# Kernel optimization log

Hardware: AMD Instinct MI355X
Metric: run time of the kernel (lower is better)

The kernel has to match this reference:

```python
import jax, jax.numpy as jnp
import numpy as np

DIM, D_STATE, D_CONV, EXPAND = 128, 16, 4, 2
D_INNER = EXPAND * DIM          # 256
DT_RANK = (DIM + 15) // 16      # 8
HIDDEN = int(DIM * 4.0)         # 512


def layer_norm(x, w, b, eps=1e-5):
    mu = x.mean(-1, keepdims=True)
    var = ((x - mu) ** 2).mean(-1, keepdims=True)
    return (x - mu) * jax.lax.rsqrt(var + eps) * w + b


def mamba(x, in_proj_w, conv_w, conv_b, x_proj_w, dt_proj_w, dt_proj_b, A_log, D, out_proj_w):
    # x: [B, L, dim]
    B, L, _ = x.shape
    xz = jnp.einsum('bld,ed->ble', x, in_proj_w)          # [B,L,2*Din]
    xc, z = jnp.split(xz, 2, axis=-1)                     # [B,L,Din] each
    # causal depthwise conv1d over L
    xcT = jnp.swapaxes(xc, 1, 2)                          # [B,Din,L]
    xcT = jax.lax.conv_general_dilated(
        xcT, conv_w, window_strides=(1,), padding=[(D_CONV - 1, 0)],
        dimension_numbers=('NCH', 'OIH', 'NCH'), feature_group_count=D_INNER)
    xc = jax.nn.silu(jnp.swapaxes(xcT, 1, 2) + conv_b)    # [B,L,Din]
    # input-dependent SSM parameters
    x_dbl = jnp.einsum('bld,ed->ble', xc, x_proj_w)       # [B,L,dt_rank+2N]
    dt, Bm, Cm = jnp.split(x_dbl, [DT_RANK, DT_RANK + D_STATE], axis=-1)
    delta = jax.nn.softplus(jnp.einsum('blr,dr->bld', dt, dt_proj_w) + dt_proj_b)  # [B,L,Din]
    A = -jnp.exp(A_log)                                   # [Din,N]
    deltaA = jnp.exp(delta[..., None] * A)                # [B,L,Din,N]
    deltaBu = (delta * xc)[..., None] * Bm[:, :, None, :] # [B,L,Din,N]
    # linear recurrence over L: h = deltaA*h + deltaBu ; y = <h, C>
    def step(h, inp):
        dA, dBu, c = inp
        h = dA * h + dBu                                  # [B,Din,N]
        return h, jnp.einsum('bdn,bn->bd', h, c)
    h0 = jnp.zeros((B, D_INNER, D_STATE), deltaA.dtype)
    _, ys = jax.lax.scan(step, h0, (jnp.swapaxes(deltaA, 0, 1),
                                    jnp.swapaxes(deltaBu, 0, 1),
                                    jnp.swapaxes(Cm, 0, 1)))
    y = jnp.swapaxes(ys, 0, 1) + xc * D                   # [B,L,Din]
    y = y * jax.nn.silu(z)
    return jnp.einsum('bld,od->blo', y, out_proj_w)       # [B,L,dim]


def mlp(x, H, W, fc1_w, fc1_b, dw_w, dw_b, fc2_w, fc2_b):
    B, L, _ = x.shape
    T = L // (H * W)
    h = jnp.einsum('bld,hd->blh', x, fc1_w) + fc1_b       # [B,L,hidden]
    hs = h.reshape(B * T, H, W, HIDDEN)                   # NHWC
    hs = jax.lax.conv_general_dilated(
        hs, dw_w, window_strides=(1, 1), padding='SAME',
        dimension_numbers=('NHWC', 'HWIO', 'NHWC'), feature_group_count=HIDDEN) + dw_b
    h = jax.nn.gelu(hs.reshape(B, L, HIDDEN), approximate=False)
    return jnp.einsum('blh,oh->blo', h, fc2_w) + fc2_b


def setup_inputs() -> dict:
    key = jax.random.key(0)
    ks = jax.random.split(key, 20)
    s = 0.02
    return {
        'x_in': jax.random.normal(ks[0], (2, 8, DIM, 32, 32), jnp.float32),
        'norm1_w': jnp.ones((DIM,), jnp.float32),
        'norm1_b': jnp.zeros((DIM,), jnp.float32),
        'in_proj_w': jax.random.normal(ks[1], (2 * D_INNER, DIM), jnp.float32) * s,
        'conv_w': jax.random.normal(ks[2], (D_INNER, 1, D_CONV), jnp.float32) * s,
        'conv_b': jnp.zeros((D_INNER,), jnp.float32),
        'x_proj_w': jax.random.normal(ks[3], (DT_RANK + 2 * D_STATE, D_INNER), jnp.float32) * s,
        'dt_proj_w': jax.random.normal(ks[4], (D_INNER, DT_RANK), jnp.float32) * s,
        'dt_proj_b': jax.random.uniform(ks[5], (D_INNER,), jnp.float32, -4.0, -2.0),
        'A_log': jnp.log(jnp.broadcast_to(jnp.arange(1, D_STATE + 1, dtype=jnp.float32), (D_INNER, D_STATE))),
        'D': jnp.ones((D_INNER,), jnp.float32),
        'out_proj_w': jax.random.normal(ks[6], (DIM, D_INNER), jnp.float32) * s,
        'norm2_w': jnp.ones((DIM,), jnp.float32),
        'norm2_b': jnp.zeros((DIM,), jnp.float32),
        'fc1_w': jax.random.normal(ks[7], (HIDDEN, DIM), jnp.float32) * s,
        'fc1_b': jnp.zeros((HIDDEN,), jnp.float32),
        'dw_w': jax.random.normal(ks[8], (3, 3, 1, HIDDEN), jnp.float32) * s,
        'dw_b': jnp.zeros((HIDDEN,), jnp.float32),
        'fc2_w': jax.random.normal(ks[9], (DIM, HIDDEN), jnp.float32) * s,
        'fc2_b': jnp.zeros((DIM,), jnp.float32),
    }


def reference(x_in, norm1_w, norm1_b, in_proj_w, conv_w, conv_b, x_proj_w,
              dt_proj_w, dt_proj_b, A_log, D, out_proj_w, norm2_w, norm2_b,
              fc1_w, fc1_b, dw_w, dw_b, fc2_w, fc2_b):
    B, T, C, H, W = x_in.shape
    L = T * H * W
    x = jnp.transpose(x_in, (0, 1, 3, 4, 2)).reshape(B, L, C)
    shortcut = x
    xn = layer_norm(x, norm1_w, norm1_b)
    mamba_args = (in_proj_w, conv_w, conv_b, x_proj_w, dt_proj_w, dt_proj_b, A_log, D, out_proj_w)
    out = mamba(xn, *mamba_args) + jnp.flip(mamba(jnp.flip(xn, 1), *mamba_args), 1)
    x = shortcut + out
    x = x + mlp(layer_norm(x, norm2_w, norm2_b), H, W, fc1_w, fc1_b, dw_w, dw_b, fc2_w, fc2_b)
    return jnp.transpose(x.reshape(B, T, H, W, C), (0, 1, 4, 2, 3))
```

## Files before the change

### kernel.cpp

```cpp
#include <hip/hip_runtime.h>
#include <math.h>

#define BB 2
#define HWSZ 1024
#define LL 8192
#define MM 16384
#define DMODEL 128
#define DIN 256
#define NST 16
#define CH 32
#define NCH 256

typedef __attribute__((ext_vector_type(8))) short bf16x8;
typedef __attribute__((ext_vector_type(4))) float f32x4;

__device__ __forceinline__ float siluf(float x){ return x/(1.f+__expf(-x)); }
__device__ __forceinline__ unsigned short f2bf(float x){
  unsigned u = __float_as_uint(x);
  unsigned r = (u + 0x7fffu + ((u>>16)&1u)) >> 16;
  return (unsigned short)r;
}
__device__ __forceinline__ float bf2f(unsigned short h){ return __uint_as_float(((unsigned)h)<<16); }
__device__ __forceinline__ float softplusf(float x){
  return fmaxf(x,0.f) + __logf(1.f + __expf(-fabsf(x)));
}

__global__ __launch_bounds__(256) void k_tln(const float* __restrict__ in,
    const float* __restrict__ w, const float* __restrict__ b,
    float* __restrict__ x_t, unsigned short* __restrict__ xn){
  __shared__ float st[128][33];
  int bt = blockIdx.y, hw0 = blockIdx.x*32;
  int t = threadIdx.x;
  int tx = t & 31, ty = t >> 5;
  #pragma unroll
  for (int j=0;j<16;j++){
    int c = ty + j*8;
    st[c][tx] = in[((size_t)(bt*DMODEL + c))*HWSZ + hw0 + tx];
  }
  __syncthreads();
  int wv = t >> 6, l = t & 63;
  float2 wgt = *(const float2*)(w + 2*l);
  float2 bia = *(const float2*)(b + 2*l);
  #pragma unroll
  for (int p=0;p<8;p++){
    int tok = p*4 + wv;
    float e0 = st[2*l][tok], e1 = st[2*l+1][tok];
    float s = e0+e1, sq = e0*e0+e1*e1;
    #pragma unroll
    for (int off=32; off>=1; off>>=1){ s += __shfl_xor(s,off); sq += __shfl_xor(sq,off); }
    float mu = s*(1.f/128.f);
    float var = sq*(1.f/128.f) - mu*mu;
    float rs = rsqrtf(var + 1e-5f);
    size_t tg = (size_t)bt*HWSZ + hw0 + tok;
    *(float2*)(x_t + tg*DMODEL + 2*l) = make_float2(e0,e1);
    ushort2 o;
    o.x = f2bf((e0-mu)*rs*wgt.x + bia.x);
    o.y = f2bf((e1-mu)*rs*wgt.y + bia.y);
    *(ushort2*)(xn + tg*DMODEL + 2*l) = o;
  }
}

__global__ void k_prep_weights(const float* __restrict__ ipw, const float* __restrict__ xpw,
                               const float* __restrict__ dtw, const float* __restrict__ opw,
                               const float* __restrict__ f1w, const float* __restrict__ f2w,
                               unsigned short* __restrict__ wb){
  int i = blockIdx.x*256 + threadIdx.x;
  const int T0=65536, T1=T0+81920, T2=T1+32768, T3=T2+65536, T4=T3+65536;
  if (i >= T4) return;
  float v;
  if (i < T0) v = ipw[i];
  else if (i < T1){
    int j = i - T0; int row = j >> 8; int col = j & 255;
    if (row < 256){
      float acc = 0.f;
      #pragma unroll
      for (int r=0;r<8;r++) acc += dtw[row*8+r]*xpw[r*256+col];
      v = acc;
    } else if (row < 288) v = xpw[(8 + row-256)*256 + col];
    else v = 0.f;
  }
  else if (i < T2) v = opw[i - T1];
  else if (i < T3) v = f1w[i - T2];
  else v = f2w[i - T3];
  wb[i] = f2bf(v);
}

template<int BM, int BN, int WM, int WN, int EPI>
__global__ __launch_bounds__(256) void k_mgemm(
    const unsigned short* __restrict__ A, const unsigned short* __restrict__ W,
    void* __restrict__ Cout, const float* __restrict__ bias,
    const float* __restrict__ add, unsigned short* __restrict__ C2,
    const float* __restrict__ lnw, const float* __restrict__ lnb,
    int M, int N, int K){
  constexpr int BK = 64;
  constexpr int TM = WM/16, TN = WN/16;
  constexpr int NWN = BN/WN;
  static_assert((BM/WM)*(BN/WN) == 4, "4 waves");
  __shared__ unsigned short As[BM*BK];
  __shared__ unsigned short Bs[BN*BK];
  const int tid = threadIdx.x;
  const int w = tid >> 6, l = tid & 63;
  const int m0 = blockIdx.y*BM, n0 = blockIdx.x*BN;
  const int wm = w / NWN, wn = w % NWN;
  f32x4 acc[TM][TN];
  #pragma unroll
  for (int i=0;i<TM;i++)
    #pragma unroll
    for (int j=0;j<TN;j++) acc[i][j] = (f32x4){0.f,0.f,0.f,0.f};
  const int lrow = l >> 3;
  const int lswz = ((l & 7) ^ lrow) * 8;
  const int rl = l & 15;
  const int gh = l >> 4;
  const int sx7 = l & 7;
  for (int k0 = 0; k0 < K; k0 += BK){
    #pragma unroll
    for (int r0 = 0; r0 < BM; r0 += 32){
      int rr = r0 + w*8;
      const unsigned short* gp = A + (size_t)(m0 + rr + lrow)*K + k0 + lswz;
      __builtin_amdgcn_global_load_lds(
        (const __attribute__((address_space(1))) unsigned int*)gp,
        (__attribute__((address_space(3))) unsigned int*)(As + rr*BK), 16, 0, 0);
    }
    #pragma unroll
    for (int r0 = 0; r0 < BN; r0 += 32){
      int rr = r0 + w*8;
      const unsigned short* gp = W + (size_t)(n0 + rr + lrow)*K + k0 + lswz;
      __builtin_amdgcn_global_load_lds(
        (const __attribute__((address_space(1))) unsigned int*)gp,
        (__attribute__((address_space(3))) unsigned int*)(Bs + rr*BK), 16, 0, 0);
    }
    __syncthreads();
    #pragma unroll
    for (int kk = 0; kk < 2; kk++){
      const int slot = ((kk*4 + gh) ^ sx7) * 8;
      bf16x8 af[TM], bfr[TN];
      #pragma unroll
      for (int i=0;i<TM;i++)
        af[i] = *(const bf16x8*)(As + (wm*WM + i*16 + rl)*BK + slot);
      #pragma unroll
      for (int j=0;j<TN;j++)
        bfr[j] = *(const bf16x8*)(Bs + (wn*WN + j*16 + rl)*BK + slot);
      #pragma unroll
      for (int i=0;i<TM;i++)
        #pragma unroll
        for (int j=0;j<TN;j++)
          acc[i][j] = __builtin_amdgcn_mfma_f32_16x16x32_bf16(af[i], bfr[j], acc[i][j], 0,0,0);
    }
    __syncthreads();
  }
  if constexpr (EPI == 5){
    __shared__ float st2[64][65];
    __syncthreads();
    #pragma unroll
    for (int i=0;i<TM;i++){
      #pragma unroll
      for (int j=0;j<TN;j++){
        #pragma unroll
        for (int r=0;r<4;r++){
          int rloc = wm*WM + i*16 + (gh<<2) + r;
          int cloc = wn*WN + j*16 + rl;
          int row = m0 + rloc, col = n0 + cloc;
          st2[rloc][cloc] = acc[i][j][r] + bias[col] + add[(size_t)row*N + col];
        }
      }
    }
    __syncthreads();
    int bt = m0 >> 10, hw0 = m0 & 1023;
    float* outp = (float*)Cout;
    #pragma unroll
    for (int it=0; it<16; it++){
      int colL = it*4 + w;
      outp[((size_t)(bt*DMODEL + n0 + colL))*HWSZ + hw0 + l] = st2[l][colL];
    }
  } else if constexpr (EPI == 6){
    __shared__ float st2[64][129];
    __syncthreads();
    #pragma unroll
    for (int i=0;i<TM;i++){
      #pragma unroll
      for (int j=0;j<TN;j++){
        #pragma unroll
        for (int r=0;r<4;r++){
          int rloc = wm*WM + i*16 + (gh<<2) + r;
          int cloc = wn*WN + j*16 + rl;
          int row = m0 + rloc;
          float v = acc[i][j][r] + add[(size_t)row*128 + cloc];
          st2[rloc][cloc] = v;
          ((float*)Cout)[(size_t)row*128 + cloc] = v;
        }
      }
    }
    __syncthreads();
    int rr = tid >> 2, part = tid & 3;
    float s = 0.f, sq = 0.f;
    #pragma unroll
    for (int q=0;q<32;q++){
      float v = st2[rr][part*32+q];
      s += v; sq += v*v;
    }
    s += __shfl_xor(s,1); s += __shfl_xor(s,2);
    sq += __shfl_xor(sq,1); sq += __shfl_xor(sq,2);
    float mu = s*(1.f/128.f);
    float var = sq*(1.f/128.f) - mu*mu;
    float rs = rsqrtf(var + 1e-5f);
    int row = m0 + rr;
    #pragma unroll
    for (int q=0;q<32;q+=2){
      int col = part*32 + q;
      ushort2 o;
      o.x = f2bf((st2[rr][col]  -mu)*rs*lnw[col]   + lnb[col]);
      o.y = f2bf((st2[rr][col+1]-mu)*rs*lnw[col+1] + lnb[col+1]);
      *(ushort2*)(C2 + (size_t)row*128 + col) = o;
    }
  } else {
    #pragma unroll
    for (int i=0;i<TM;i++){
      #pragma unroll
      for (int j=0;j<TN;j++){
        #pragma unroll
        for (int r=0;r<4;r++){
          int row = m0 + wm*WM + i*16 + (gh<<2) + r;
          int col = n0 + wn*WN + j*16 + rl;
          float v = acc[i][j][r];
          if (EPI == 0){
            ((unsigned short*)Cout)[(size_t)row*N + col] = f2bf(v);
          } else if (EPI == 1){
            ((unsigned short*)Cout)[(size_t)row*N + col] = f2bf(v + bias[col]);
          } else if (EPI == 2){
            if (col < 256){
              ((unsigned short*)Cout)[(size_t)row*256 + col] = f2bf(softplusf(v + bias[col]));
            } else if (col < 288){
              C2[(size_t)row*32 + (col-256)] = f2bf(v);
            }
          } else if (EPI == 3){
            ((float*)Cout)[(size_t)row*N + col] = v + add[(size_t)row*N + col];
          }
        }
      }
    }
  }
}

__global__ void k_conv1d(const unsigned short* __restrict__ xz, const float* __restrict__ cw,
                         const float* __restrict__ cb, unsigned short* __restrict__ xcf,
                         unsigned short* __restrict__ xcb){
  int idx = blockIdx.x*256 + threadIdx.x;
  int d4 = (idx & 63)*4;
  int ml = idx >> 6;
  int b = ml >> 13, l = ml & (LL-1);
  float4 t0 = *(const float4*)(cw + (size_t)(d4+0)*4);
  float4 t1 = *(const float4*)(cw + (size_t)(d4+1)*4);
  float4 t2 = *(const float4*)(cw + (size_t)(d4+2)*4);
  float4 t3 = *(const float4*)(cw + (size_t)(d4+3)*4);
  float wk[4][4];
  wk[0][0]=t0.x; wk[1][0]=t0.y; wk[2][0]=t0.z; wk[3][0]=t0.w;
  wk[0][1]=t1.x; wk[1][1]=t1.y; wk[2][1]=t1.z; wk[3][1]=t1.w;
  wk[0][2]=t2.x; wk[1][2]=t2.y; wk[2][2]=t2.z; wk[3][2]=t2.w;
  wk[0][3]=t3.x; wk[1][3]=t3.y; wk[2][3]=t3.z; wk[3][3]=t3.w;
  float4 bv = *(const float4*)(cb + d4);
  const unsigned short* base = xz + (size_t)b*LL*512 + d4;
  float4 af = {0,0,0,0};
  #pragma unroll
  for (int k=0;k<4;k++){
    int lp = l-3+k;
    if (lp>=0){
      ushort4 u = *(const ushort4*)(base + (size_t)lp*512);
      af.x += wk[k][0]*bf2f(u.x); af.y += wk[k][1]*bf2f(u.y);
      af.z += wk[k][2]*bf2f(u.z); af.w += wk[k][3]*bf2f(u.w);
    }
  }
  ushort4 of;
  of.x = f2bf(siluf(af.x+bv.x)); of.y = f2bf(siluf(af.y+bv.y));
  of.z = f2bf(siluf(af.z+bv.z)); of.w = f2bf(siluf(af.w+bv.w));
  *(ushort4*)(xcf + (size_t)ml*DIN + d4) = of;
  float4 ab = {0,0,0,0};
  #pragma unroll
  for (int k=0;k<4;k++){
    int lp = l+3-k;
    if (lp<LL){
      ushort4 u = *(const ushort4*)(base + (size_t)lp*512);
      ab.x += wk[k][0]*bf2f(u.x); ab.y += wk[k][1]*bf2f(u.y);
      ab.z += wk[k][2]*bf2f(u.z); ab.w += wk[k][3]*bf2f(u.w);
    }
  }
  ushort4 ob;
  ob.x = f2bf(siluf(ab.x+bv.x)); ob.y = f2bf(siluf(ab.y+bv.y));
  ob.z = f2bf(siluf(ab.z+bv.z)); ob.w = f2bf(siluf(ab.w+bv.w));
  *(ushort4*)(xcb + (size_t)ml*DIN + d4) = ob;
}

__global__ __launch_bounds__(256) void k_scan_ph1(
    const unsigned short* __restrict__ df, const unsigned short* __restrict__ db,
    const unsigned short* __restrict__ xf, const unsigned short* __restrict__ xb,
    const unsigned short* __restrict__ bcf, const unsigned short* __restrict__ bcb,
    float* __restrict__ ssum_buf, float* __restrict__ sHH){
  int c = blockIdx.x, b = blockIdx.y, dir = blockIdx.z;
  int d = threadIdx.x;
  const unsigned short* delta = dir? db : df;
  const unsigned short* xc = dir? xb : xf;
  const unsigned short* bc = dir? bcb : bcf;
  __shared__ float sb[8][32];
  float h[NST];
  #pragma unroll
  for (int n=0;n<NST;n++) h[n]=0.f;
  float ssum = 0.f;
  size_t rowbase = (size_t)b*LL;
  for (int s0=0;s0<CH;s0+=8){
    __syncthreads();
    {
      int i = d>>5, j = d&31;
      int step = s0+i;
      int l = dir ? (c*CH + CH-1-step) : (c*CH + step);
      sb[i][j] = bf2f(bc[(rowbase + l)*32 + j]);
    }
    __syncthreads();
    #pragma unroll
    for (int i=0;i<8;i++){
      int step = s0+i;
      int l = dir ? (c*CH + CH-1-step) : (c*CH + step);
      size_t ro = (rowbase + l)*DIN + d;
      float dlt = bf2f(delta[ro]);
      float xv  = bf2f(xc[ro]);
      float du = dlt*xv;
      float r = __expf(-dlt);
      ssum += dlt;
      float rp = 1.f;
      #pragma unroll
      for (int n=0;n<NST;n++){
        rp *= r;
        h[n] = rp*h[n] + du*sb[i][n];
      }
    }
  }
  size_t bd = (size_t)b*2 + dir;
  ssum_buf[(bd*NCH + c)*DIN + d] = ssum;
  size_t sb2 = ((bd*NCH + c)*DIN + d)*NST;
  #pragma unroll
  for (int n=0;n<NST;n+=4)
    *(float4*)(sHH + sb2 + n) = make_float4(h[n],h[n+1],h[n+2],h[n+3]);
}

__global__ void k_scan_ph2a(const float* __restrict__ ssum_buf, const float* __restrict__ sHH,
                            float* __restrict__ hg, float* __restrict__ ssg){
  int gid = blockIdx.x*256 + threadIdx.x;
  int dn = gid & 4095;
  int rest = gid >> 12;
  int g = rest & 15, bd = rest >> 4;
  int dir = bd & 1;
  int d = dn >> 4, n = dn & 15;
  float np1 = -(float)(n+1);
  float run = 0.f, ss = 0.f;
  size_t base = (size_t)bd*NCH*4096 + dn;
  size_t sbase = (size_t)bd*NCH*DIN + d;
  #pragma unroll
  for (int s=0;s<16;s++){
    int p = g*16 + s;
    int c = dir ? (NCH-1-p) : p;
    float sv = ssum_buf[sbase + (size_t)c*DIN];
    float Pv = __expf(np1*sv);
    run = Pv*run + sHH[base + (size_t)c*4096];
    ss += sv;
  }
  hg[((size_t)bd*16 + g)*4096 + dn] = run;
  if (n == 0) ssg[((size_t)bd*16 + g)*DIN + d] = ss;
}

__global__ void k_scan_ph2b(const float* __restrict__ ssg, const float* __restrict__ hg,
                            float* __restrict__ Rbuf){
  int gid = blockIdx.x*256 + threadIdx.x;
  int dn = gid & 4095; int bd = gid >> 12;
  int d = dn >> 4, n = dn & 15;
  float np1 = -(float)(n+1);
  float run = 0.f;
  #pragma unroll
  for (int g=0; g<16; g++){
    size_t gi = (size_t)bd*16 + g;
    float Pg = __expf(np1 * ssg[gi*DIN + d]);
    float hgv = hg[gi*4096 + dn];
    Rbuf[gi*4096 + dn] = run;
    run = Pg*run + hgv;
  }
}

__global__ void k_scan_ph2c(const float* __restrict__ ssum_buf, const float* __restrict__ Rbuf,
                            float* __restrict__ sHH){
  int gid = blockIdx.x*256 + threadIdx.x;
  int dn = gid & 4095;
  int rest = gid >> 12;
  int g = rest & 15, bd = rest >> 4;
  int dir = bd & 1;
  int d = dn >> 4, n = dn & 15;
  float np1 = -(float)(n+1);
  float run = Rbuf[((size_t)bd*16 + g)*4096 + dn];
  size_t base = (size_t)bd*NCH*4096 + dn;
  size_t sbase = (size_t)bd*NCH*DIN + d;
  #pragma unroll
  for (int s=0;s<16;s++){
    int p = g*16 + s;
    int c = dir ? (NCH-1-p) : p;
    float Pv = __expf(np1 * ssum_buf[sbase + (size_t)c*DIN]);
    size_t idx = base + (size_t)c*4096;
    float hl = sHH[idx];
    sHH[idx] = run;
    run = Pv*run + hl;
  }
}

__global__ __launch_bounds__(128) void k_scan_ph3(
    const unsigned short* __restrict__ df, const unsigned short* __restrict__ db,
    const unsigned short* __restrict__ xf, const unsigned short* __restrict__ xb,
    const unsigned short* __restrict__ bcf, const unsigned short* __restrict__ bcb,
    const float* __restrict__ sHH, const unsigned short* __restrict__ xz,
    const float* __restrict__ Dp, unsigned short* __restrict__ yc){
  int c = blockIdx.x, b = blockIdx.y;
  int t = threadIdx.x;
  int d = blockIdx.z*128 + t;
  __shared__ float sb[8][32];
  __shared__ float sy[CH][128];
  float Dv = Dp[d];
  size_t rowbase = (size_t)b*LL;
  float h[NST];
  {
    size_t hb = ((((size_t)b*2 + 0)*NCH + c)*DIN + d)*NST;
    #pragma unroll
    for (int n=0;n<NST;n+=4){
      float4 v = *(const float4*)(sHH + hb + n);
      h[n]=v.x; h[n+1]=v.y; h[n+2]=v.z; h[n+3]=v.w;
    }
  }
  for (int s0=0;s0<CH;s0+=8){
    __syncthreads();
    for (int e=t;e<256;e+=128){
      int i = e>>5, j = e&31;
      int l = c*CH + s0 + i;
      sb[i][j] = bf2f(bcf[(rowbase + l)*32 + j]);
    }
    __syncthreads();
    #pragma unroll
    for (int i=0;i<8;i++){
      int p = s0+i;
      size_t ro = (rowbase + c*CH + p)*DIN + d;
      float dlt = bf2f(df[ro]);
      float xv  = bf2f(xf[ro]);
      float du = dlt*xv;
      float r = __expf(-dlt);
      float y = 0.f, rp = 1.f;
      #pragma unroll
      for (int n=0;n<NST;n++){
        rp *= r;
        h[n] = rp*h[n] + du*sb[i][n];
        y += h[n]*sb[i][16+n];
      }
      sy[p][t] = y + xv*Dv;
    }
  }
  {
    size_t hb = ((((size_t)b*2 + 1)*NCH + c)*DIN + d)*NST;
    #pragma unroll
    for (int n=0;n<NST;n+=4){
      float4 v = *(const float4*)(sHH + hb + n);
      h[n]=v.x; h[n+1]=v.y; h[n+2]=v.z; h[n+3]=v.w;
    }
  }
  for (int s0=0;s0<CH;s0+=8){
    __syncthreads();
    for (int e=t;e<256;e+=128){
      int i = e>>5, j = e&31;
      int l = c*CH + CH-1-(s0+i);
      sb[i][j] = bf2f(bcb[(rowbase + l)*32 + j]);
    }
    __syncthreads();
    #pragma unroll
    for (int i=0;i<8;i++){
      int p = CH-1-(s0+i);
      int l = c*CH + p;
      size_t ro = (rowbase + l)*DIN + d;
      float dlt = bf2f(db[ro]);
      float xv  = bf2f(xb[ro]);
      float du = dlt*xv;
      float r = __expf(-dlt);
      float y = 0.f, rp = 1.f;
      #pragma unroll
      for (int n=0;n<NST;n++){
        rp *= r;
        h[n] = rp*h[n] + du*sb[i][n];
        y += h[n]*sb[i][16+n];
      }
      float tot = sy[p][t] + y + xv*Dv;
      float z = bf2f(xz[(rowbase + l)*512 + 256 + d]);
      yc[(rowbase + l)*DIN + d] = f2bf(tot * siluf(z));
    }
  }
}

__global__ void k_dwconv(const unsigned short* __restrict__ hin, const float* __restrict__ w3,
                         const float* __restrict__ b3, unsigned short* __restrict__ hout){
  int idx = blockIdx.x*256 + threadIdx.x;
  int c4 = (idx & 127)*4;
  int ml = idx >> 7;
  int slab = ml >> 10; int hw = ml & 1023; int hh = hw >> 5, ww = hw & 31;
  float4 acc = *(const float4*)(b3 + c4);
  #pragma unroll
  for (int dy=-1; dy<=1; dy++){
    int h2 = hh+dy; if (h2<0||h2>=32) continue;
    #pragma unroll
    for (int dx=-1; dx<=1; dx++){
      int w2 = ww+dx; if (w2<0||w2>=32) continue;
      ushort4 u = *(const ushort4*)(hin + ((size_t)slab*HWSZ + h2*32 + w2)*512 + c4);
      float4 wt = *(const float4*)(w3 + (size_t)((dy+1)*3 + (dx+1))*512 + c4);
      acc.x += bf2f(u.x)*wt.x; acc.y += bf2f(u.y)*wt.y;
      acc.z += bf2f(u.z)*wt.z; acc.w += bf2f(u.w)*wt.w;
    }
  }
  ushort4 o;
  o.x = f2bf(0.5f*acc.x*(1.f+erff(acc.x*0.70710678118f)));
  o.y = f2bf(0.5f*acc.y*(1.f+erff(acc.y*0.70710678118f)));
  o.z = f2bf(0.5f*acc.z*(1.f+erff(acc.z*0.70710678118f)));
  o.w = f2bf(0.5f*acc.w*(1.f+erff(acc.w*0.70710678118f)));
  *(ushort4*)(hout + (size_t)ml*512 + c4) = o;
}

extern "C" void kernel_launch(void* const* d_in, const int* in_sizes, int n_in,
                              void* d_out, int out_size, void* d_ws, size_t ws_size,
                              hipStream_t stream){
  const float* x_in      = (const float*)d_in[0];
  const float* n1w       = (const float*)d_in[1];
  const float* n1b       = (const float*)d_in[2];
  const float* in_proj_w = (const float*)d_in[3];
  const float* conv_w    = (const float*)d_in[4];
  const float* conv_b    = (const float*)d_in[5];
  const float* x_proj_w  = (const float*)d_in[6];
  const float* dt_proj_w = (const float*)d_in[7];
  const float* dt_proj_b = (const float*)d_in[8];
  const float* Dp        = (const float*)d_in[10];
  const float* out_proj_w= (const float*)d_in[11];
  const float* n2w       = (const float*)d_in[12];
  const float* n2b       = (const float*)d_in[13];
  const float* fc1_w     = (const float*)d_in[14];
  const float* fc1_b     = (const float*)d_in[15];
  const float* dw_w      = (const float*)d_in[16];
  const float* dw_b      = (const float*)d_in[17];
  const float* fc2_w     = (const float*)d_in[18];
  const float* fc2_b     = (const float*)d_in[19];

  char* ws = (char*)d_ws;
  float* x_t  = (float*)ws;                                   ws += (size_t)MM*128*4;
  unsigned short* xn  = (unsigned short*)ws;                  ws += (size_t)MM*128*2;
  unsigned short* xz  = (unsigned short*)ws;                  ws += (size_t)MM*512*2;
  unsigned short* xcf = (unsigned short*)ws;                  ws += (size_t)MM*256*2;
  unsigned short* xcb = (unsigned short*)ws;                  ws += (size_t)MM*256*2;
  unsigned short* df  = (unsigned short*)ws;                  ws += (size_t)MM*256*2;
  unsigned short* db  = (unsigned short*)ws;                  ws += (size_t)MM*256*2;
  unsigned short* bcf = (unsigned short*)ws;                  ws += (size_t)MM*32*2;
  unsigned short* bcb = (unsigned short*)ws;                  ws += (size_t)MM*32*2;
  unsigned short* yc  = (unsigned short*)ws;                  ws += (size_t)MM*256*2;
  unsigned short* wb  = (unsigned short*)ws;                  ws += 311296*2;
  float* ssum = (float*)ws;                                   ws += (size_t)4*NCH*DIN*4;
  float* hg   = (float*)ws;                                   ws += (size_t)4*16*4096*4;
  float* ssg  = (float*)ws;                                   ws += (size_t)4*16*DIN*4;
  float* Rbuf = (float*)ws;                                   ws += (size_t)4*16*4096*4;
  float* sH   = (float*)ws;                                   ws += (size_t)4*NCH*4096*4;
  float* x2   = sH;

  unsigned short* wb_ip = wb;
  unsigned short* wb_w2 = wb + 65536;
  unsigned short* wb_op = wb + 65536 + 81920;
  unsigned short* wb_f1 = wb + 65536 + 81920 + 32768;
  unsigned short* wb_f2 = wb + 65536 + 81920 + 32768 + 65536;

  k_prep_weights<<<1216,256,0,stream>>>(in_proj_w, x_proj_w, dt_proj_w, out_proj_w, fc1_w, fc2_w, wb);
  k_tln<<<dim3(32,16),256,0,stream>>>(x_in, n1w, n1b, x_t, xn);
  k_mgemm<128,128,64,64,0><<<dim3(4, MM/128),256,0,stream>>>(xn, wb_ip, xz, nullptr, nullptr, nullptr, nullptr, nullptr, MM, 512, 128);
  k_conv1d<<<MM*64/256,256,0,stream>>>(xz, conv_w, conv_b, xcf, xcb);
  k_mgemm<64,64,32,32,2><<<dim3(5, 2*MM/64),256,0,stream>>>(xcf, wb_w2, df, dt_proj_b, nullptr, bcf, nullptr, nullptr, 2*MM, 320, 256);
  k_scan_ph1<<<dim3(NCH,BB,2),256,0,stream>>>(df,db,xcf,xcb,bcf,bcb,ssum,sH);
  k_scan_ph2a<<<1024,256,0,stream>>>(ssum,sH,hg,ssg);
  k_scan_ph2b<<<64,256,0,stream>>>(ssg,hg,Rbuf);
  k_scan_ph2c<<<1024,256,0,stream>>>(ssum,Rbuf,sH);
  k_scan_ph3<<<dim3(NCH,BB,2),128,0,stream>>>(df,db,xcf,xcb,bcf,bcb,sH,xz,Dp,yc);
  k_mgemm<64,128,32,64,6><<<dim3(1, MM/64),256,0,stream>>>(yc, wb_op, x2, nullptr, x_t, xn, n2w, n2b, MM, 128, 256);
  k_mgemm<128,128,64,64,1><<<dim3(4, MM/128),256,0,stream>>>(xn, wb_f1, xz, fc1_b, nullptr, nullptr, nullptr, nullptr, MM, 512, 128);
  k_dwconv<<<MM*128/256,256,0,stream>>>(xz, dw_w, dw_b, xcf);
  k_mgemm<64,64,32,32,5><<<dim3(2, MM/64),256,0,stream>>>(xcf, wb_f2, d_out, fc2_b, x2, nullptr, nullptr, nullptr, MM, 128, 512);
}
```

Baseline: 262.4 us.

## Run both scan directions in parallel in ph3, store chunk states as bf16

The final scan kernel now processes forward and backward directions concurrently in the two halves of a 256-thread block, combining them through shared memory before the gated output write. Chunk-boundary states passed between scan phases are stored in bf16 instead of fp32 to halve their memory traffic. The serial power chain for exp(-delta)^n is replaced with a shallower multiplication tree. The bf16 states introduce extra rounding in carried states, and the larger blocks and shared buffers raise resource use per block.

```diff
diff --git a/kernel.cpp b/kernel.cpp
--- a/kernel.cpp
+++ b/kernel.cpp
@@ -23,6 +23,13 @@
 __device__ __forceinline__ float bf2f(unsigned short h){ return __uint_as_float(((unsigned)h)<<16); }
 __device__ __forceinline__ float softplusf(float x){
   return fmaxf(x,0.f) + __logf(1.f + __expf(-fabsf(x)));
+}
+__device__ __forceinline__ void pow_tree(float r, float* q){
+  float r2 = r*r, r4 = r2*r2, r8 = r4*r4;
+  q[0]=r;      q[1]=r2;     q[2]=r2*r;   q[3]=r4;
+  q[4]=r4*r;   q[5]=r4*r2;  q[6]=r4*q[2];q[7]=r8;
+  q[8]=r8*r;   q[9]=r8*r2;  q[10]=r8*q[2];q[11]=r8*r4;
+  q[12]=r8*q[4];q[13]=r8*q[5];q[14]=r8*q[6];q[15]=r8*r8;
 }
 
 __global__ __launch_bounds__(256) void k_tln(const float* __restrict__ in,
@@ -293,7 +300,7 @@
     const unsigned short* __restrict__ df, const unsigned short* __restrict__ db,
     const unsigned short* __restrict__ xf, const unsigned short* __restrict__ xb,
     const unsigned short* __restrict__ bcf, const unsigned short* __restrict__ bcb,
-    float* __restrict__ ssum_buf, float* __restrict__ sHH){
+    float* __restrict__ ssum_buf, unsigned short* __restrict__ sHH){
   int c = blockIdx.x, b = blockIdx.y, dir = blockIdx.z;
   int d = threadIdx.x;
   const unsigned short* delta = dir? db : df;
@@ -324,23 +331,24 @@
       float du = dlt*xv;
       float r = __expf(-dlt);
       ssum += dlt;
-      float rp = 1.f;
-      #pragma unroll
-      for (int n=0;n<NST;n++){
-        rp *= r;
-        h[n] = rp*h[n] + du*sb[i][n];
-      }
+      float q[NST];
+      pow_tree(r, q);
+      #pragma unroll
+      for (int n=0;n<NST;n++) h[n] = q[n]*h[n] + du*sb[i][n];
     }
   }
   size_t bd = (size_t)b*2 + dir;
   ssum_buf[(bd*NCH + c)*DIN + d] = ssum;
   size_t sb2 = ((bd*NCH + c)*DIN + d)*NST;
   #pragma unroll
-  for (int n=0;n<NST;n+=4)
-    *(float4*)(sHH + sb2 + n) = make_float4(h[n],h[n+1],h[n+2],h[n+3]);
-}
-
-__global__ void k_scan_ph2a(const float* __restrict__ ssum_buf, const float* __restrict__ sHH,
+  for (int n=0;n<NST;n+=4){
+    ushort4 o;
+    o.x = f2bf(h[n]); o.y = f2bf(h[n+1]); o.z = f2bf(h[n+2]); o.w = f2bf(h[n+3]);
+    *(ushort4*)(sHH + sb2 + n) = o;
+  }
+}
+
+__global__ void k_scan_ph2a(const float* __restrict__ ssum_buf, const unsigned short* __restrict__ sHH,
                             float* __restrict__ hg, float* __restrict__ ssg){
   int gid = blockIdx.x*256 + threadIdx.x;
   int dn = gid & 4095;
@@ -358,7 +366,7 @@
     int c = dir ? (NCH-1-p) : p;
     float sv = ssum_buf[sbase + (size_t)c*DIN];
     float Pv = __expf(np1*sv);
-    run = Pv*run + sHH[base + (size_t)c*4096];
+    run = Pv*run + bf2f(sHH[base + (size_t)c*4096]);
     ss += sv;
   }
   hg[((size_t)bd*16 + g)*4096 + dn] = run;
@@ -383,7 +391,7 @@
 }
 
 __global__ void k_scan_ph2c(const float* __restrict__ ssum_buf, const float* __restrict__ Rbuf,
-                            float* __restrict__ sHH){
+                            unsigned short* __restrict__ sHH){
   int gid = blockIdx.x*256 + threadIdx.x;
   int dn = gid & 4095;
   int rest = gid >> 12;
@@ -400,96 +408,78 @@
     int c = dir ? (NCH-1-p) : p;
     float Pv = __expf(np1 * ssum_buf[sbase + (size_t)c*DIN]);
     size_t idx = base + (size_t)c*4096;
-    float hl = sHH[idx];
-    sHH[idx] = run;
+    float hl = bf2f(sHH[idx]);
+    sHH[idx] = f2bf(run);
     run = Pv*run + hl;
   }
 }
 
-__global__ __launch_bounds__(128) void k_scan_ph3(
+__global__ __launch_bounds__(256) void k_scan_ph3(
     const unsigned short* __restrict__ df, const unsigned short* __restrict__ db,
     const unsigned short* __restrict__ xf, const unsigned short* __restrict__ xb,
     const unsigned short* __restrict__ bcf, const unsigned short* __restrict__ bcb,
-    const float* __restrict__ sHH, const unsigned short* __restrict__ xz,
+    const unsigned short* __restrict__ sHH, const unsigned short* __restrict__ xz,
     const float* __restrict__ Dp, unsigned short* __restrict__ yc){
-  int c = blockIdx.x, b = blockIdx.y;
+  int c = blockIdx.x, b = blockIdx.y, dh = blockIdx.z;
   int t = threadIdx.x;
-  int d = blockIdx.z*128 + t;
-  __shared__ float sb[8][32];
-  __shared__ float sy[CH][128];
+  int half = t >> 7;
+  int td = t & 127;
+  int d = dh*128 + td;
+  __shared__ float sbf[8][32], sbb[8][32];
+  __shared__ float syf[CH][128], syb[CH][128];
   float Dv = Dp[d];
   size_t rowbase = (size_t)b*LL;
+  const unsigned short* dl  = half? db  : df;
+  const unsigned short* xl  = half? xb  : xf;
+  const unsigned short* bcl = half? bcb : bcf;
+  float (*sbp)[32] = half? sbb : sbf;
+  float (*syp)[128] = half? syb : syf;
   float h[NST];
   {
-    size_t hb = ((((size_t)b*2 + 0)*NCH + c)*DIN + d)*NST;
+    size_t hb = ((((size_t)b*2 + half)*NCH + c)*DIN + d)*NST;
     #pragma unroll
     for (int n=0;n<NST;n+=4){
-      float4 v = *(const float4*)(sHH + hb + n);
-      h[n]=v.x; h[n+1]=v.y; h[n+2]=v.z; h[n+3]=v.w;
+      ushort4 v = *(const ushort4*)(sHH + hb + n);
+      h[n]=bf2f(v.x); h[n+1]=bf2f(v.y); h[n+2]=bf2f(v.z); h[n+3]=bf2f(v.w);
     }
   }
   for (int s0=0;s0<CH;s0+=8){
     __syncthreads();
-    for (int e=t;e<256;e+=128){
+    #pragma unroll
+    for (int e=td; e<256; e+=128){
       int i = e>>5, j = e&31;
-      int l = c*CH + s0 + i;
-      sb[i][j] = bf2f(bcf[(rowbase + l)*32 + j]);
+      int l = half ? (c*CH + CH-1-(s0+i)) : (c*CH + s0+i);
+      sbp[i][j] = bf2f(bcl[(rowbase + l)*32 + j]);
     }
     __syncthreads();
     #pragma unroll
     for (int i=0;i<8;i++){
-      int p = s0+i;
+      int p = half ? (CH-1-(s0+i)) : (s0+i);
       size_t ro = (rowbase + c*CH + p)*DIN + d;
-      float dlt = bf2f(df[ro]);
-      float xv  = bf2f(xf[ro]);
+      float dlt = bf2f(dl[ro]);
+      float xv  = bf2f(xl[ro]);
       float du = dlt*xv;
       float r = __expf(-dlt);
-      float y = 0.f, rp = 1.f;
+      float q[NST];
+      pow_tree(r, q);
+      float y = 0.f;
       #pragma unroll
       for (int n=0;n<NST;n++){
-        rp *= r;
-        h[n] = rp*h[n] + du*sb[i][n];
-        y += h[n]*sb[i][16+n];
+        h[n] = q[n]*h[n] + du*sbp[i][n];
+        y += h[n]*sbp[i][16+n];
       }
-      sy[p][t] = y + xv*Dv;
-    }
-  }
-  {
-    size_t hb = ((((size_t)b*2 + 1)*NCH + c)*DIN + d)*NST;
-    #pragma unroll
-    for (int n=0;n<NST;n+=4){
-      float4 v = *(const float4*)(sHH + hb + n);
-      h[n]=v.x; h[n+1]=v.y; h[n+2]=v.z; h[n+3]=v.w;
-    }
-  }
-  for (int s0=0;s0<CH;s0+=8){
-    __syncthreads();
-    for (int e=t;e<256;e+=128){
-      int i = e>>5, j = e&31;
-      int l = c*CH + CH-1-(s0+i);
-      sb[i][j] = bf2f(bcb[(rowbase + l)*32 + j]);
-    }
-    __syncthreads();
-    #pragma unroll
-    for (int i=0;i<8;i++){
-      int p = CH-1-(s0+i);
-      int l = c*CH + p;
-      size_t ro = (rowbase + l)*DIN + d;
-      float dlt = bf2f(db[ro]);
-      float xv  = bf2f(xb[ro]);
-      float du = dlt*xv;
-      float r = __expf(-dlt);
-      float y = 0.f, rp = 1.f;
-      #pragma unroll
-      for (int n=0;n<NST;n++){
-        rp *= r;
-        h[n] = rp*h[n] + du*sb[i][n];
-        y += h[n]*sb[i][16+n];
-      }
-      float tot = sy[p][t] + y + xv*Dv;
-      float z = bf2f(xz[(rowbase + l)*512 + 256 + d]);
-      yc[(rowbase + l)*DIN + d] = f2bf(tot * siluf(z));
-    }
+      syp[p][td] = y + xv*Dv;
+    }
+  }
+  __syncthreads();
+  #pragma unroll
+  for (int e=t; e<CH*128; e+=256){
+    int p = e>>7, tc = e&127;
+    int l = c*CH + p;
+    int dd = dh*128 + tc;
+    float tot = syf[p][tc] + syb[p][tc];
+    float z = bf2f(xz[(rowbase + l)*512 + 256 + dd]);
+    yc[(rowbase + l)*DIN + dd] = f2bf(tot * siluf(z));
   }
 }
 
@@ -559,8 +549,8 @@
   float* hg   = (float*)ws;                                   ws += (size_t)4*16*4096*4;
   float* ssg  = (float*)ws;                                   ws += (size_t)4*16*DIN*4;
   float* Rbuf = (float*)ws;                                   ws += (size_t)4*16*4096*4;
-  float* sH   = (float*)ws;                                   ws += (size_t)4*NCH*4096*4;
-  float* x2   = sH;
+  unsigned short* sH = (unsigned short*)ws;                   ws += (size_t)4*NCH*4096*2;
+  float* x2   = (float*)sH;
 
   unsigned short* wb_ip = wb;
   unsigned short* wb_w2 = wb + 65536;
@@ -577,7 +567,7 @@
   k_scan_ph2a<<<1024,256,0,stream>>>(ssum,sH,hg,ssg);
   k_scan_ph2b<<<64,256,0,stream>>>(ssg,hg,Rbuf);
   k_scan_ph2c<<<1024,256,0,stream>>>(ssum,Rbuf,sH);
-  k_scan_ph3<<<dim3(NCH,BB,2),128,0,stream>>>(df,db,xcf,xcb,bcf,bcb,sH,xz,Dp,yc);
+  k_scan_ph3<<<dim3(NCH,BB,2),256,0,stream>>>(df,db,xcf,xcb,bcf,bcb,sH,xz,Dp,yc);
   k_mgemm<64,128,32,64,6><<<dim3(1, MM/64),256,0,stream>>>(yc, wb_op, x2, nullptr, x_t, xn, n2w, n2b, MM, 128, 256);
   k_mgemm<128,128,64,64,1><<<dim3(4, MM/128),256,0,stream>>>(xn, wb_f1, xz, fc1_b, nullptr, nullptr, nullptr, nullptr, MM, 512, 128);
   k_dwconv<<<MM*128/256,256,0,stream>>>(xz, dw_w, dw_b, xcf);
```

After: 332.2 us. 26.6% more time.
